# Kernel optimization log

Hardware: AMD Instinct MI355X
Metric: run time of the kernel (lower is better)

## Reference

```python
import jax, jax.numpy as jnp
import numpy as np

D_MODEL, D_FF, N_EXPERTS, TOP_K = 1024, 4096, 8, 2
LN_EPS = 1e-5


def setup_inputs() -> dict:
    key = jax.random.key(0)
    ks = jax.random.split(key, 9)
    s = 0.02
    return {
        "x": jax.random.normal(ks[0], (4, 2048, D_MODEL), dtype=jnp.float32),
        "Wg": jax.random.normal(ks[1], (D_MODEL, N_EXPERTS), dtype=jnp.float32) * s,
        "bg": jnp.zeros((N_EXPERTS,), dtype=jnp.float32),
        "W1": jax.random.normal(ks[2], (N_EXPERTS, D_MODEL, D_FF), dtype=jnp.float32) * s,
        "b1": jnp.zeros((N_EXPERTS, D_FF), dtype=jnp.float32),
        "W2": jax.random.normal(ks[3], (N_EXPERTS, D_FF, D_MODEL), dtype=jnp.float32) * s,
        "b2": jnp.zeros((N_EXPERTS, D_MODEL), dtype=jnp.float32),
        "gamma": jnp.ones((D_MODEL,), dtype=jnp.float32),
        "beta": jnp.zeros((D_MODEL,), dtype=jnp.float32),
    }


def _moe(x, Wg, bg, W1, b1, W2, b2, gamma, beta):
    B, S, D = x.shape
    xf = x.reshape(B * S, D)                       # (T, D)
    logits = xf @ Wg + bg                          # (T, E)
    probs = jax.nn.softmax(logits, axis=-1)
    topk_scores, topk_idx = jax.lax.top_k(probs, TOP_K)   # (T, K)
    # combine weights per expert: w[t, e] = sum_k score[t,k] * [idx[t,k]==e]
    onehot = jax.nn.one_hot(topk_idx, N_EXPERTS, dtype=probs.dtype)  # (T, K, E)
    w = jnp.einsum("tk,tke->te", topk_scores, onehot)                # (T, E)
    # load-balancing aux loss (switch-style): E * sum_e f_e * P_e
    f = jnp.mean(onehot, axis=(0, 1)) * 1.0        # fraction of routed slots per expert
    P = jnp.mean(probs, axis=0)
    aux_loss = jnp.float32(N_EXPERTS) * jnp.sum(f * P)
    # dense-equivalent expert compute; zero weight for unrouted tokens matches
    # the masked gather/scatter math of the original.
    out = jnp.zeros_like(xf)
    for e in range(N_EXPERTS):
        h = jax.nn.relu(xf @ W1[e] + b1[e])        # (T, D_FF)
        y = h @ W2[e] + b2[e]                      # (T, D)
        out = out + w[:, e:e + 1] * y
    out = out.reshape(B, S, D)
    # residual + post-layernorm (dropout disabled, eval mode)
    z = x + out
    mu = jnp.mean(z, axis=-1, keepdims=True)
    var = jnp.mean(jnp.square(z - mu), axis=-1, keepdims=True)
    z = (z - mu) * jax.lax.rsqrt(var + LN_EPS) * gamma + beta
    return z, aux_loss


def reference(x, Wg, bg, W1, b1, W2, b2, gamma, beta):
    return _moe(x, Wg, bg, W1, b1, W2, b2, gamma, beta)
```

## Files before the change

### kernel.cpp

```cpp
#include <hip/hip_runtime.h>

#define T_TOK 8192
#define DM    1024
#define DFF   4096
#define NE    8
#define CAP   2560
#define SLOTS (NE * CAP)
#define MTILES 20

typedef __attribute__((ext_vector_type(4))) float f32x4;
typedef __attribute__((ext_vector_type(8))) short bf16x8;
typedef __attribute__((ext_vector_type(4))) unsigned short u16x4;

__device__ __forceinline__ unsigned short f2bf(float f) {
  unsigned int u = __float_as_uint(f);
  u = (u + 0x7FFFu + ((u >> 16) & 1u)) >> 16;
  return (unsigned short)u;
}
__device__ __forceinline__ float bf2f(unsigned short u) {
  return __uint_as_float(((unsigned)u) << 16);
}

__device__ __forceinline__ void gld_lds16(const void* g, void* l) {
  __builtin_amdgcn_global_load_lds(
      (const __attribute__((address_space(1))) void*)g,
      (__attribute__((address_space(3))) void*)l, 16, 0, 0);
}

__device__ __forceinline__ bf16x8 ldsr(unsigned addr) {
  bf16x8 r;
  asm volatile("ds_read_b128 %0, %1" : "=v"(r) : "v"(addr));
  return r;
}

__global__ __launch_bounds__(256) void transpose_convert2(
    const float* __restrict__ W1, unsigned short* __restrict__ W1t,
    const float* __restrict__ W2, unsigned short* __restrict__ W2t)
{
  __shared__ float tile[64][65];
  int z = blockIdx.z;
  const float* W; unsigned short* Wt; int R, C, c0, r0;
  if (z < 8) {
    W = W1 + (size_t)z * DM * DFF; Wt = W1t + (size_t)z * DM * DFF;
    R = DM; C = DFF;
    c0 = blockIdx.x * 64; r0 = blockIdx.y * 64;
  } else {
    W = W2 + (size_t)(z - 8) * DM * DFF; Wt = W2t + (size_t)(z - 8) * DM * DFF;
    R = DFF; C = DM;
    c0 = (blockIdx.x & 15) * 64; r0 = (blockIdx.y * 4 + (blockIdx.x >> 4)) * 64;
  }
  int tid = threadIdx.x;
  int lr = tid >> 4, lc = (tid & 15) * 4;
#pragma unroll
  for (int i = 0; i < 4; ++i) {
    float4 v = *(const float4*)(W + (size_t)(r0 + i * 16 + lr) * C + c0 + lc);
    tile[i * 16 + lr][lc] = v.x; tile[i * 16 + lr][lc + 1] = v.y;
    tile[i * 16 + lr][lc + 2] = v.z; tile[i * 16 + lr][lc + 3] = v.w;
  }
  __syncthreads();
#pragma unroll
  for (int i = 0; i < 4; ++i) {
    int o = i * 256 + tid;
    int rq = o & 15, cw = o >> 4;
    u16x4 u;
    u.x = f2bf(tile[rq * 4 + 0][cw]); u.y = f2bf(tile[rq * 4 + 1][cw]);
    u.z = f2bf(tile[rq * 4 + 2][cw]); u.w = f2bf(tile[rq * 4 + 3][cw]);
    __builtin_nontemporal_store(u, (u16x4*)(Wt + (size_t)(c0 + cw) * R + r0 + rq * 4));
  }
}

__global__ __launch_bounds__(256) void router_kernel(
    const float* __restrict__ x, const float* __restrict__ Wg, const float* __restrict__ bg,
    int* __restrict__ slotOf, float* __restrict__ slot_w,
    int* __restrict__ pos, float* __restrict__ P_sh,
    unsigned short* __restrict__ Abuf)
{
  __shared__ float wgT[NE * DM];
  for (int i = threadIdx.x; i < NE * DM; i += 256) {
    int d = i >> 3, e = i & 7;
    wgT[e * DM + d] = Wg[i];
  }
  __syncthreads();
  int w = threadIdx.x >> 6, lane = threadIdx.x & 63;
  int sh = blockIdx.x & 63;
  for (int it = 0; it < 4; ++it) {
    int t = (blockIdx.x * 4 + w) * 4 + it;
    float4 xv[4];
    float p[NE];
#pragma unroll
    for (int e = 0; e < NE; ++e) p[e] = 0.f;
#pragma unroll
    for (int ps = 0; ps < 4; ++ps) {
      int d0 = ps * 256 + lane * 4;
      xv[ps] = *(const float4*)(x + (size_t)t * DM + d0);
#pragma unroll
      for (int e = 0; e < NE; ++e) {
        float4 wv = *(const float4*)(wgT + e * DM + d0);
        p[e] += xv[ps].x * wv.x + xv[ps].y * wv.y + xv[ps].z * wv.z + xv[ps].w * wv.w;
      }
    }
#pragma unroll
    for (int e = 0; e < NE; ++e) {
#pragma unroll
      for (int o = 1; o < 64; o <<= 1) p[e] += __shfl_xor(p[e], o);
      p[e] += bg[e];
    }
    float mx = p[0];
#pragma unroll
    for (int e = 1; e < NE; ++e) mx = fmaxf(mx, p[e]);
    float se = 0.f;
#pragma unroll
    for (int e = 0; e < NE; ++e) { p[e] = expf(p[e] - mx); se += p[e]; }
    float inv = 1.f / se;
#pragma unroll
    for (int e = 0; e < NE; ++e) p[e] *= inv;
    int e0 = 0; float v0 = p[0];
#pragma unroll
    for (int e = 1; e < NE; ++e) if (p[e] > v0) { v0 = p[e]; e0 = e; }
    int e1 = -1; float v1 = -1.f;
#pragma unroll
    for (int e = 0; e < NE; ++e) if (e != e0 && p[e] > v1) { v1 = p[e]; e1 = e; }
    int p0 = 0, p1 = 0;
    if (lane == 0) {
      p0 = atomicAdd(&pos[e0], 1);
      p1 = atomicAdd(&pos[e1], 1);
    }
    p0 = __shfl(p0, 0); p1 = __shfl(p1, 0);
    int s0 = e0 * CAP + (p0 < CAP ? p0 : CAP - 1);
    int s1 = e1 * CAP + (p1 < CAP ? p1 : CAP - 1);
    if (lane == 0) {
      slotOf[2 * t] = s0; slotOf[2 * t + 1] = s1;
      slot_w[s0] = v0; slot_w[s1] = v1;
#pragma unroll
      for (int e = 0; e < NE; ++e) atomicAdd(&P_sh[sh * 8 + e], p[e]);
    }
    unsigned short* d0p = Abuf + (size_t)s0 * DM;
    unsigned short* d1p = Abuf + (size_t)s1 * DM;
#pragma unroll
    for (int ps = 0; ps < 4; ++ps) {
      int d = ps * 256 + lane * 4;
      ushort4 u;
      u.x = f2bf(xv[ps].x); u.y = f2bf(xv[ps].y);
      u.z = f2bf(xv[ps].z); u.w = f2bf(xv[ps].w);
      *(ushort4*)(d0p + d) = u;
      *(ushort4*)(d1p + d) = u;
    }
  }
}

template<int KDIM, int EPI>
__global__ __launch_bounds__(256, 3) void moe_gemm(
    const unsigned short* __restrict__ A, const unsigned short* __restrict__ Bt,
    const float* __restrict__ bias, unsigned short* __restrict__ Out,
    const int* __restrict__ pos, const float* __restrict__ slot_w, int N)
{
  constexpr int KT = (EPI == 0 ? KDIM : KDIM / 2) / 32;
  int e, koff, sp;
  if (EPI == 0) { e = blockIdx.z; koff = 0; sp = 0; }
  else { e = blockIdx.z >> 1; sp = blockIdx.z & 1; koff = sp * (KDIM / 2); }

  int cnt = pos[e];
  if (cnt > CAP) cnt = CAP;

  int nx = N >> 7;
  int b = blockIdx.x + blockIdx.y * nx;
  int cpx = nx * MTILES / 8;
  int wg = (b & 7) * cpx + (b >> 3);
  int ntile = wg / MTILES, mt = wg % MTILES;
  if (mt * 128 >= cnt) return;
  int m0 = e * CAP + mt * 128, n0 = ntile * 128;

  __shared__ __align__(16) char lds[49152];

  const int tid = threadIdx.x, lane = tid & 63, w = tid >> 6;
  const int wr = w >> 1, wc = w & 1;

  const int ssl = 8 * ((tid & 3) ^ ((tid >> 3) & 3));
  const unsigned short* Asrc = A + (size_t)(m0 + (tid >> 2)) * KDIM + koff + ssl;
  const unsigned short* Bsrc = Bt + (size_t)e * N * KDIM + (size_t)(n0 + (tid >> 2)) * KDIM + koff + ssl;

  unsigned lbase = (unsigned)(size_t)(__attribute__((address_space(3))) char*)lds;
  const unsigned swz = 16u * (unsigned)((lane >> 4) ^ ((lane >> 1) & 3));
  const unsigned aoff = (unsigned)((wr * 64 + (lane & 15)) * 64) + swz;
  const unsigned boff = 8192u + (unsigned)((wc * 64 + (lane & 15)) * 64) + swz;

  f32x4 acc[4][4] = {};
  bf16x8 Aq[4], Bq[4];

#define STAGE(KT_, BUFO_)                                                    \
  { int k0_ = (KT_) * 32;                                                    \
    char* lb_ = lds + (BUFO_);                                               \
    gld_lds16(Asrc + k0_,                      lb_ + tid * 16);              \
    gld_lds16(Asrc + (size_t)64 * KDIM + k0_,  lb_ + 4096 + tid * 16);       \
    gld_lds16(Bsrc + k0_,                      lb_ + 8192 + tid * 16);       \
    gld_lds16(Bsrc + (size_t)64 * KDIM + k0_,  lb_ + 12288 + tid * 16); }

  STAGE(0, 0)
  STAGE(1, 16384)
  asm volatile("s_waitcnt vmcnt(4)" ::: "memory");
  __builtin_amdgcn_s_barrier();

  unsigned cur = 0;
#pragma unroll 1
  for (int kt = 0; kt < KT; ++kt) {
    unsigned bo = lbase + cur;
    if (kt + 2 < KT) {
      unsigned stg = cur + 32768u; if (stg >= 49152u) stg -= 49152u;
      STAGE(kt + 2, stg)
    }
#pragma unroll
    for (int mi = 0; mi < 4; ++mi) Aq[mi] = ldsr(bo + aoff + mi * 1024u);
#pragma unroll
    for (int ni = 0; ni < 4; ++ni) Bq[ni] = ldsr(bo + boff + ni * 1024u);
    asm volatile("s_waitcnt lgkmcnt(0)" ::: "memory");
    __builtin_amdgcn_sched_barrier(0);
    __builtin_amdgcn_s_setprio(1);
#pragma unroll
    for (int mi = 0; mi < 4; ++mi)
#pragma unroll
      for (int ni = 0; ni < 4; ++ni)
        acc[mi][ni] = __builtin_amdgcn_mfma_f32_16x16x32_bf16(
            Aq[mi], Bq[ni], acc[mi][ni], 0, 0, 0);
    __builtin_amdgcn_s_setprio(0);
    if (kt + 2 < KT)      asm volatile("s_waitcnt vmcnt(4)" ::: "memory");
    else if (kt + 1 < KT) asm volatile("s_waitcnt vmcnt(0)" ::: "memory");
    __builtin_amdgcn_s_barrier();
    cur += 16384u; if (cur == 49152u) cur = 0;
  }
#undef STAGE

  int cn = lane & 15;
  int r4 = (lane >> 4) * 4;
  if (EPI == 0) {
#pragma unroll
    for (int ni = 0; ni < 4; ++ni) {
      int col = n0 + wc * 64 + ni * 16 + cn;
      float bv = bias[e * N + col];
#pragma unroll
      for (int mi = 0; mi < 4; ++mi) {
        int row = m0 + wr * 64 + mi * 16 + r4;
#pragma unroll
        for (int j = 0; j < 4; ++j) {
          float v = acc[mi][ni][j] + bv;
          __builtin_nontemporal_store(f2bf(v > 0.f ? v : 0.f),
                                      Out + (size_t)(row + j) * N + col);
        }
      }
    }
  } else {
    unsigned short* Yw = Out + (size_t)sp * SLOTS * DM;
    float bv[4];
#pragma unroll
    for (int ni = 0; ni < 4; ++ni)
      bv[ni] = (sp == 0) ? bias[e * N + n0 + wc * 64 + ni * 16 + cn] : 0.f;
#pragma unroll
    for (int mi = 0; mi < 4; ++mi) {
      int rbase = m0 + wr * 64 + mi * 16 + r4;
#pragma unroll
      for (int j = 0; j < 4; ++j) {
        int slot = rbase + j;
        float wgt = slot_w[slot];
#pragma unroll
        for (int ni = 0; ni < 4; ++ni) {
          int col = n0 + wc * 64 + ni * 16 + cn;
          __builtin_nontemporal_store(f2bf(wgt * (acc[mi][ni][j] + bv[ni])),
                                      Yw + (size_t)slot * DM + col);
        }
      }
    }
  }
}

__global__ __launch_bounds__(256) void ln_kernel(
    const float* __restrict__ x, const unsigned short* __restrict__ Ybuf,
    const int* __restrict__ slotOf,
    const float* __restrict__ gamma, const float* __restrict__ beta,
    float* __restrict__ out)
{
  int t = blockIdx.x;
  int s0 = slotOf[2 * t], s1 = slotOf[2 * t + 1];
  const unsigned short* y00 = Ybuf + (size_t)s0 * DM;
  const unsigned short* y01 = Ybuf + (size_t)SLOTS * DM + (size_t)s0 * DM;
  const unsigned short* y10 = Ybuf + (size_t)s1 * DM;
  const unsigned short* y11 = Ybuf + (size_t)SLOTS * DM + (size_t)s1 * DM;
  int c = threadIdx.x * 4;
  float4 xv = *(const float4*)(x + (size_t)t * DM + c);
  ushort4 a0 = *(const ushort4*)(y00 + c);
  ushort4 a1 = *(const ushort4*)(y01 + c);
  ushort4 a2 = *(const ushort4*)(y10 + c);
  ushort4 a3 = *(const ushort4*)(y11 + c);
  float z[4];
  z[0] = xv.x + bf2f(a0.x) + bf2f(a1.x) + bf2f(a2.x) + bf2f(a3.x);
  z[1] = xv.y + bf2f(a0.y) + bf2f(a1.y) + bf2f(a2.y) + bf2f(a3.y);
  z[2] = xv.z + bf2f(a0.z) + bf2f(a1.z) + bf2f(a2.z) + bf2f(a3.z);
  z[3] = xv.w + bf2f(a0.w) + bf2f(a1.w) + bf2f(a2.w) + bf2f(a3.w);
  float s = z[0] + z[1] + z[2] + z[3];
  float s2 = z[0]*z[0] + z[1]*z[1] + z[2]*z[2] + z[3]*z[3];
#pragma unroll
  for (int o = 1; o < 64; o <<= 1) { s += __shfl_xor(s, o); s2 += __shfl_xor(s2, o); }
  __shared__ float ls[8];
  int w = threadIdx.x >> 6, lane = threadIdx.x & 63;
  if (lane == 0) { ls[w] = s; ls[4 + w] = s2; }
  __syncthreads();
  s = ls[0] + ls[1] + ls[2] + ls[3];
  s2 = ls[4] + ls[5] + ls[6] + ls[7];
  float mu = s * (1.f / DM);
  float var = s2 * (1.f / DM) - mu * mu;
  float rstd = rsqrtf(var + 1e-5f);
  float4 gv = *(const float4*)(gamma + c);
  float4 bv = *(const float4*)(beta + c);
  float4 ov;
  ov.x = (z[0] - mu) * rstd * gv.x + bv.x;
  ov.y = (z[1] - mu) * rstd * gv.y + bv.y;
  ov.z = (z[2] - mu) * rstd * gv.z + bv.z;
  ov.w = (z[3] - mu) * rstd * gv.w + bv.w;
  *(float4*)(out + (size_t)t * DM + c) = ov;
}

__global__ void aux_kernel(const float* __restrict__ P_sh,
                           const int* __restrict__ pos, float* __restrict__ out_aux)
{
  if (threadIdx.x == 0) {
    float aux = 0.f;
    for (int e = 0; e < NE; ++e) {
      float P = 0.f;
      for (int i = 0; i < 64; ++i) P += P_sh[i * 8 + e];
      P *= (1.f / T_TOK);
      float f = pos[e] * (1.f / (T_TOK * 2));
      aux += f * P;
    }
    out_aux[0] = (float)NE * aux;
  }
}

extern "C" void kernel_launch(void* const* d_in, const int* in_sizes, int n_in,
                              void* d_out, int out_size, void* d_ws, size_t ws_size,
                              hipStream_t stream)
{
  (void)in_sizes; (void)n_in; (void)out_size; (void)ws_size;
  const float* x     = (const float*)d_in[0];
  const float* Wg    = (const float*)d_in[1];
  const float* bg    = (const float*)d_in[2];
  const float* W1    = (const float*)d_in[3];
  const float* b1    = (const float*)d_in[4];
  const float* W2    = (const float*)d_in[5];
  const float* b2    = (const float*)d_in[6];
  const float* gamma = (const float*)d_in[7];
  const float* beta  = (const float*)d_in[8];
  float* out = (float*)d_out;

  char* ws = (char*)d_ws;
  size_t off = 0;
  auto alloc = [&](size_t bytes) -> void* {
    void* p = ws + off;
    off += (bytes + 255) & ~(size_t)255;
    return p;
  };
  int*   pos      = (int*)alloc(8 * 4);
  float* P_sh     = (float*)alloc(64 * 8 * 4);
  size_t meta_end = off;
  int*   slotOf   = (int*)alloc(16384 * 4);
  float* slot_w   = (float*)alloc((size_t)SLOTS * 4);
  unsigned short* Hbuf = (unsigned short*)alloc((size_t)SLOTS * DFF * 2);
  unsigned short* W2t  = (unsigned short*)alloc((size_t)NE * DM * DFF * 2);
  unsigned short* Abuf = (unsigned short*)alloc((size_t)SLOTS * DM * 2);
  unsigned short* W1t  = (unsigned short*)alloc((size_t)2 * SLOTS * DM * 2);
  unsigned short* Ybuf = W1t;

  (void)hipMemsetAsync(d_ws, 0, meta_end, stream);

  transpose_convert2<<<dim3(64, 16, 16), 256, 0, stream>>>(W1, W1t, W2, W2t);
  router_kernel<<<512, 256, 0, stream>>>(x, Wg, bg, slotOf, slot_w, pos, P_sh, Abuf);
  moe_gemm<DM, 0><<<dim3(32, MTILES, 8), 256, 0, stream>>>(
      Abuf, W1t, b1, Hbuf, pos, slot_w, DFF);
  moe_gemm<DFF, 1><<<dim3(8, MTILES, 16), 256, 0, stream>>>(
      Hbuf, W2t, b2, Ybuf, pos, slot_w, DM);
  ln_kernel<<<T_TOK, 256, 0, stream>>>(x, Ybuf, slotOf, gamma, beta, out);
  aux_kernel<<<1, 64, 0, stream>>>(P_sh, pos, out + (size_t)T_TOK * DM);
}
```

Baseline: 727.4 us.

## Merge weight transpose with router kernel and pipeline LDS reads with MFMA

```diff
diff --git a/kernel.cpp b/kernel.cpp
--- a/kernel.cpp
+++ b/kernel.cpp
@@ -33,58 +33,59 @@
   return r;
 }
 
-__global__ __launch_bounds__(256) void transpose_convert2(
+__global__ __launch_bounds__(256) void prep_kernel(
     const float* __restrict__ W1, unsigned short* __restrict__ W1t,
-    const float* __restrict__ W2, unsigned short* __restrict__ W2t)
-{
-  __shared__ float tile[64][65];
-  int z = blockIdx.z;
-  const float* W; unsigned short* Wt; int R, C, c0, r0;
-  if (z < 8) {
-    W = W1 + (size_t)z * DM * DFF; Wt = W1t + (size_t)z * DM * DFF;
-    R = DM; C = DFF;
-    c0 = blockIdx.x * 64; r0 = blockIdx.y * 64;
-  } else {
-    W = W2 + (size_t)(z - 8) * DM * DFF; Wt = W2t + (size_t)(z - 8) * DM * DFF;
-    R = DFF; C = DM;
-    c0 = (blockIdx.x & 15) * 64; r0 = (blockIdx.y * 4 + (blockIdx.x >> 4)) * 64;
-  }
+    const float* __restrict__ W2, unsigned short* __restrict__ W2t,
+    const float* __restrict__ x, const float* __restrict__ Wg, const float* __restrict__ bg,
+    unsigned short* __restrict__ Abuf,
+    int* __restrict__ slotOf, float* __restrict__ slot_w,
+    int* __restrict__ pos, float* __restrict__ P_sh)
+{
+  __shared__ __align__(16) char smem[32768];
   int tid = threadIdx.x;
-  int lr = tid >> 4, lc = (tid & 15) * 4;
-#pragma unroll
-  for (int i = 0; i < 4; ++i) {
-    float4 v = *(const float4*)(W + (size_t)(r0 + i * 16 + lr) * C + c0 + lc);
-    tile[i * 16 + lr][lc] = v.x; tile[i * 16 + lr][lc + 1] = v.y;
-    tile[i * 16 + lr][lc + 2] = v.z; tile[i * 16 + lr][lc + 3] = v.w;
-  }
-  __syncthreads();
-#pragma unroll
-  for (int i = 0; i < 4; ++i) {
-    int o = i * 256 + tid;
-    int rq = o & 15, cw = o >> 4;
-    u16x4 u;
-    u.x = f2bf(tile[rq * 4 + 0][cw]); u.y = f2bf(tile[rq * 4 + 1][cw]);
-    u.z = f2bf(tile[rq * 4 + 2][cw]); u.w = f2bf(tile[rq * 4 + 3][cw]);
-    __builtin_nontemporal_store(u, (u16x4*)(Wt + (size_t)(c0 + cw) * R + r0 + rq * 4));
-  }
-}
-
-__global__ __launch_bounds__(256) void router_kernel(
-    const float* __restrict__ x, const float* __restrict__ Wg, const float* __restrict__ bg,
-    int* __restrict__ slotOf, float* __restrict__ slot_w,
-    int* __restrict__ pos, float* __restrict__ P_sh,
-    unsigned short* __restrict__ Abuf)
-{
-  __shared__ float wgT[NE * DM];
-  for (int i = threadIdx.x; i < NE * DM; i += 256) {
+  if (blockIdx.x < 16384) {
+    float (*tile)[65] = (float(*)[65])smem;
+    int bx = blockIdx.x & 63, by = (blockIdx.x >> 6) & 15, z = blockIdx.x >> 10;
+    const float* W; unsigned short* Wt; int R, C, c0, r0;
+    if (z < 8) {
+      W = W1 + (size_t)z * DM * DFF; Wt = W1t + (size_t)z * DM * DFF;
+      R = DM; C = DFF;
+      c0 = bx * 64; r0 = by * 64;
+    } else {
+      W = W2 + (size_t)(z - 8) * DM * DFF; Wt = W2t + (size_t)(z - 8) * DM * DFF;
+      R = DFF; C = DM;
+      c0 = (bx & 15) * 64; r0 = (by * 4 + (bx >> 4)) * 64;
+    }
+    int lr = tid >> 4, lc = (tid & 15) * 4;
+#pragma unroll
+    for (int i = 0; i < 4; ++i) {
+      float4 v = *(const float4*)(W + (size_t)(r0 + i * 16 + lr) * C + c0 + lc);
+      tile[i * 16 + lr][lc] = v.x; tile[i * 16 + lr][lc + 1] = v.y;
+      tile[i * 16 + lr][lc + 2] = v.z; tile[i * 16 + lr][lc + 3] = v.w;
+    }
+    __syncthreads();
+#pragma unroll
+    for (int i = 0; i < 4; ++i) {
+      int o = i * 256 + tid;
+      int rq = o & 15, cw = o >> 4;
+      u16x4 u;
+      u.x = f2bf(tile[rq * 4 + 0][cw]); u.y = f2bf(tile[rq * 4 + 1][cw]);
+      u.z = f2bf(tile[rq * 4 + 2][cw]); u.w = f2bf(tile[rq * 4 + 3][cw]);
+      __builtin_nontemporal_store(u, (u16x4*)(Wt + (size_t)(c0 + cw) * R + r0 + rq * 4));
+    }
+    return;
+  }
+  float* wgT = (float*)smem;
+  int rid = blockIdx.x - 16384;
+  for (int i = tid; i < NE * DM; i += 256) {
     int d = i >> 3, e = i & 7;
     wgT[e * DM + d] = Wg[i];
   }
   __syncthreads();
-  int w = threadIdx.x >> 6, lane = threadIdx.x & 63;
-  int sh = blockIdx.x & 63;
+  int w = tid >> 6, lane = tid & 63;
+  int sh = rid & 63;
   for (int it = 0; it < 4; ++it) {
-    int t = (blockIdx.x * 4 + w) * 4 + it;
+    int t = (rid * 4 + w) * 4 + it;
     float4 xv[4];
     float p[NE];
 #pragma unroll
@@ -195,6 +196,11 @@
     gld_lds16(Bsrc + k0_,                      lb_ + 8192 + tid * 16);       \
     gld_lds16(Bsrc + (size_t)64 * KDIM + k0_,  lb_ + 12288 + tid * 16); }
 
+#define MMROW(MI)                                                            \
+  { _Pragma("unroll") for (int ni = 0; ni < 4; ++ni)                         \
+      acc[MI][ni] = __builtin_amdgcn_mfma_f32_16x16x32_bf16(                 \
+          Aq[MI], Bq[ni], acc[MI][ni], 0, 0, 0); }
+
   STAGE(0, 0)
   STAGE(1, 16384)
   asm volatile("s_waitcnt vmcnt(4)" ::: "memory");
@@ -208,19 +214,25 @@
       unsigned stg = cur + 32768u; if (stg >= 49152u) stg -= 49152u;
       STAGE(kt + 2, stg)
     }
-#pragma unroll
-    for (int mi = 0; mi < 4; ++mi) Aq[mi] = ldsr(bo + aoff + mi * 1024u);
+    Aq[0] = ldsr(bo + aoff);
 #pragma unroll
     for (int ni = 0; ni < 4; ++ni) Bq[ni] = ldsr(bo + boff + ni * 1024u);
+    Aq[1] = ldsr(bo + aoff + 1024u);
+    Aq[2] = ldsr(bo + aoff + 2048u);
+    Aq[3] = ldsr(bo + aoff + 3072u);
+    __builtin_amdgcn_s_setprio(1);
+    asm volatile("s_waitcnt lgkmcnt(3)" ::: "memory");
+    __builtin_amdgcn_sched_barrier(0);
+    MMROW(0)
+    asm volatile("s_waitcnt lgkmcnt(2)" ::: "memory");
+    __builtin_amdgcn_sched_barrier(0);
+    MMROW(1)
+    asm volatile("s_waitcnt lgkmcnt(1)" ::: "memory");
+    __builtin_amdgcn_sched_barrier(0);
+    MMROW(2)
     asm volatile("s_waitcnt lgkmcnt(0)" ::: "memory");
     __builtin_amdgcn_sched_barrier(0);
-    __builtin_amdgcn_s_setprio(1);
-#pragma unroll
-    for (int mi = 0; mi < 4; ++mi)
-#pragma unroll
-      for (int ni = 0; ni < 4; ++ni)
-        acc[mi][ni] = __builtin_amdgcn_mfma_f32_16x16x32_bf16(
-            Aq[mi], Bq[ni], acc[mi][ni], 0, 0, 0);
+    MMROW(3)
     __builtin_amdgcn_s_setprio(0);
     if (kt + 2 < KT)      asm volatile("s_waitcnt vmcnt(4)" ::: "memory");
     else if (kt + 1 < KT) asm volatile("s_waitcnt vmcnt(0)" ::: "memory");
@@ -228,6 +240,7 @@
     cur += 16384u; if (cur == 49152u) cur = 0;
   }
 #undef STAGE
+#undef MMROW
 
   int cn = lane & 15;
   int r4 = (lane >> 4) * 4;
@@ -361,16 +374,16 @@
   size_t meta_end = off;
   int*   slotOf   = (int*)alloc(16384 * 4);
   float* slot_w   = (float*)alloc((size_t)SLOTS * 4);
+  unsigned short* Abuf = (unsigned short*)alloc((size_t)SLOTS * DM * 2);
   unsigned short* Hbuf = (unsigned short*)alloc((size_t)SLOTS * DFF * 2);
   unsigned short* W2t  = (unsigned short*)alloc((size_t)NE * DM * DFF * 2);
-  unsigned short* Abuf = (unsigned short*)alloc((size_t)SLOTS * DM * 2);
   unsigned short* W1t  = (unsigned short*)alloc((size_t)2 * SLOTS * DM * 2);
   unsigned short* Ybuf = W1t;
 
   (void)hipMemsetAsync(d_ws, 0, meta_end, stream);
 
-  transpose_convert2<<<dim3(64, 16, 16), 256, 0, stream>>>(W1, W1t, W2, W2t);
-  router_kernel<<<512, 256, 0, stream>>>(x, Wg, bg, slotOf, slot_w, pos, P_sh, Abuf);
+  prep_kernel<<<16896, 256, 0, stream>>>(W1, W1t, W2, W2t, x, Wg, bg,
+                                         Abuf, slotOf, slot_w, pos, P_sh);
   moe_gemm<DM, 0><<<dim3(32, MTILES, 8), 256, 0, stream>>>(
       Abuf, W1t, b1, Hbuf, pos, slot_w, DFF);
   moe_gemm<DFF, 1><<<dim3(8, MTILES, 16), 256, 0, stream>>>(
```

Result: no change. 723.4 us (-0.6%).
